# Kernel tuning notes

Hardware: AMD Instinct MI355X
Metric: run time of the kernel (lower is better)

## Reference

```python
import jax, jax.numpy as jnp
import numpy as np

N = 131072        # total points
NUM_SEG = 128     # number of point clouds / segments
INC = 3
HID = 128
OUTC = 128
NUM_LAYER = 6
NUM_INNER = 2
EPS = 1e-3        # ACN eps
CLAMP_MIN = 1e-3  # clamp(min=0.001) on normalizer


def setup_inputs() -> dict:
    key = jax.random.key(0)
    ks = jax.random.split(key, 10)
    s = 0.05
    x = jax.random.normal(ks[0], (N, INC), dtype=jnp.float32)
    segment_idx = jnp.sort(jax.random.randint(ks[1], (N,), 0, NUM_SEG, dtype=jnp.int32))
    weight_pri = jax.random.uniform(ks[2], (N,), dtype=jnp.float32)
    Win0 = jax.random.normal(ks[3], (INC, HID), dtype=jnp.float32) * s
    bin0 = jnp.zeros((HID,), jnp.float32)
    Win_rest = jax.random.normal(ks[4], (4, HID, HID), dtype=jnp.float32) * s
    bin_rest = jnp.zeros((4, HID), jnp.float32)
    # 6 ResBlocks x 2 inner ConvLayers: Linear(128,128) + ACN(att Linear(128,1)) + relu
    conv_W = jax.random.normal(ks[5], (NUM_LAYER, NUM_INNER, HID, HID), dtype=jnp.float32) * s
    conv_b = jnp.zeros((NUM_LAYER, NUM_INNER, HID), jnp.float32)
    att_W = jax.random.normal(ks[6], (NUM_LAYER, NUM_INNER, HID, 1), dtype=jnp.float32) * s
    att_b = jnp.zeros((NUM_LAYER, NUM_INNER, 1), jnp.float32)
    # output Mlp: Linear(128,128)+lrelu, Linear(128,128)
    out_W = jax.random.normal(ks[7], (2, HID, OUTC), dtype=jnp.float32) * s
    out_b = jnp.zeros((2, OUTC), jnp.float32)
    return dict(x=x, segment_idx=segment_idx, weight_pri=weight_pri,
                Win0=Win0, bin0=bin0, Win_rest=Win_rest, bin_rest=bin_rest,
                conv_W=conv_W, conv_b=conv_b, att_W=att_W, att_b=att_b,
                out_W=out_W, out_b=out_b)


def _seg_sum(v, seg):
    return jax.ops.segment_sum(v, seg, num_segments=NUM_SEG)


def _scatter_softmax(att, seg):
    # stable softmax within segments; att: [N, 1]
    m = jax.ops.segment_max(att, seg, num_segments=NUM_SEG)
    e = jnp.exp(att - m[seg])
    return e / _seg_sum(e, seg)[seg]


def _acn(x, aw, ab, seg, wp):
    # attentive context normalization; x: [N, HID]
    a = _scatter_softmax(x @ aw + ab, seg)          # [N, 1]
    a = a * wp[:, None]
    a = a / jnp.clip(_seg_sum(a, seg)[seg], CLAMP_MIN)
    mean = _seg_sum(x * a, seg)[seg]
    out = x - mean
    std = jnp.sqrt(_seg_sum(a * out * out, seg)[seg] + EPS)
    return out / std, a


def reference(x, segment_idx, weight_pri, Win0, bin0, Win_rest, bin_rest,
              conv_W, conv_b, att_W, att_b, out_W, out_b):
    lrelu = jax.nn.leaky_relu  # slope 0.01, matches nn.LeakyReLU default
    # input Mlp + outer leaky_relu in Acne.forward
    h = lrelu(x @ Win0 + bin0)
    for i in range(3):
        h = lrelu(h @ Win_rest[i] + bin_rest[i])
    h = h @ Win_rest[3] + bin_rest[3]
    h = lrelu(h)
    last_a = None
    for li in range(NUM_LAYER):
        xin = h
        for j in range(NUM_INNER):
            xin = xin @ conv_W[li, j] + conv_b[li, j]
            xin, last_a = _acn(xin, att_W[li, j], att_b[li, j], segment_idx, weight_pri)
            xin = jax.nn.relu(xin)
        h = xin + h  # residual
    h = lrelu(h @ out_W[0] + out_b[0])
    h = h @ out_W[1] + out_b[1]
    return h, last_a
```

## Files before the change

kernel.cpp:

```cpp
#include <hip/hip_runtime.h>
#include <hip/hip_cooperative_groups.h>

namespace cg = cooperative_groups;

#define N_PTS 131072
#define NSEG 128
#define SW 132
#define PSTRIDE 33024

typedef unsigned short u16;
typedef __attribute__((ext_vector_type(8))) short short8;
typedef __attribute__((ext_vector_type(8))) unsigned short ushort8;
typedef __attribute__((ext_vector_type(4))) float f32x4;

__device__ __forceinline__ float b2f(u16 u){union{unsigned v;float f;}x;x.v=((unsigned)u)<<16;return x.f;}
__device__ __forceinline__ u16 f2b(float f){unsigned u=__float_as_uint(f);u+=0x7FFFu+((u>>16)&1u);return (u16)(u>>16);}
__device__ __forceinline__ float aload(const float* p){ return __hip_atomic_load(p, __ATOMIC_RELAXED, __HIP_MEMORY_SCOPE_AGENT); }
__device__ __forceinline__ void astore(float* p, float v){ __hip_atomic_store(p, v, __ATOMIC_RELAXED, __HIP_MEMORY_SCOPE_AGENT); }

__global__ __launch_bounds__(256) void k_wpack(const float* __restrict__ Wr,
    const float* __restrict__ convW, const float* __restrict__ outW,
    const float* __restrict__ attW, const float* __restrict__ attb,
    const float* __restrict__ convb,
    u16* __restrict__ Wf, float* __restrict__ uAtt, float* __restrict__ cAtt){
  int mat = blockIdx.x;
  const float* W = (mat<4) ? (Wr+mat*16384) : (mat<16) ? (convW+(mat-4)*16384) : (outW+(mat-16)*16384);
  u16* dst = Wf + mat*16384;
  for (int t = threadIdx.x; t < 16384; t += 256){ int n=t>>7,k=t&127; dst[t]=f2b(W[k*128+n]); }
  if (mat>=4 && mat<16){
    int l = mat-4;
    __syncthreads();
    int tid = threadIdx.x;
    if (tid < 128){
      float s = 0.f;
      for (int c=0;c<128;c++) s += b2f(dst[c*128+tid]) * attW[l*128+c];
      uAtt[l*128+tid] = s;
    } else if (tid == 128){
      float s = attb[l];
      for (int c=0;c<128;c++) s += convb[l*128+c] * attW[l*128+c];
      cAtt[l] = s;
    }
  }
}

__device__ __forceinline__ void gemm_lrelu_inplace(u16* Xs, const u16* __restrict__ Wm,
    const float* __restrict__ Bv, int wave, int q, int m16){
  short8 bfr[2][4];
  const int cA = wave*32 + 2*m16;
  #pragma unroll
  for (int ct=0; ct<2; ct++){
    int n = cA + ct;
    #pragma unroll
    for (int kc=0; kc<4; kc++) bfr[ct][kc] = *(const short8*)&Wm[n*128 + kc*32 + q*8];
  }
  const float b0 = Bv[cA], b1 = Bv[cA+1];
  #pragma unroll
  for (int rt=0; rt<8; rt++){
    const int r0 = rt*16;
    f32x4 a0={0,0,0,0}, a1={0,0,0,0};
    short8 afn = *(const short8*)&Xs[(r0+m16)*SW + q*8];
    #pragma unroll
    for (int kc=0; kc<4; kc++){
      short8 afc = afn;
      if (kc<3) afn = *(const short8*)&Xs[(r0+m16)*SW + (kc+1)*32 + q*8];
      a0 = __builtin_amdgcn_mfma_f32_16x16x32_bf16(afc, bfr[0][kc], a0, 0,0,0);
      a1 = __builtin_amdgcn_mfma_f32_16x16x32_bf16(afc, bfr[1][kc], a1, 0,0,0);
    }
    __syncthreads();
    #pragma unroll
    for (int t=0; t<4; t++){
      int rloc = r0 + q*4 + t;
      float v0 = a0[t]+b0, v1 = a1[t]+b1;
      v0 = v0>0.f ? v0 : 0.01f*v0;
      v1 = v1>0.f ? v1 : 0.01f*v1;
      *(unsigned*)&Xs[rloc*SW + cA] = (unsigned)f2b(v0) | ((unsigned)f2b(v1)<<16);
    }
  }
}

__global__ __launch_bounds__(256, 4) void k_fused(
    const float* __restrict__ x, const int* __restrict__ seg, const float* __restrict__ wp,
    const float* __restrict__ Win0, const float* __restrict__ bin0,
    const float* __restrict__ br, const float* __restrict__ convb, const float* __restrict__ outb,
    const u16* __restrict__ Wf, const float* __restrict__ uAtt, const float* __restrict__ cAtt,
    float* __restrict__ Pstat, float* __restrict__ Of, float* __restrict__ a_out)
{
  __shared__ u16 Xs[128*SW];
  __shared__ float rowP[128];
  __shared__ float eS[128], aS[128];
  __shared__ int   sgS[128];
  __shared__ float wpS[128];
  __shared__ float MhL[2][128], ScL[2][128];

  const int tid=threadIdx.x, wave=tid>>6, lane=tid&63, q=lane>>4, m16=lane&15;
  const int row0=blockIdx.x*128;
  const int c8=(tid*8)&127;
  const int rbase=tid>>4;

  cg::grid_group grid = cg::this_grid();

  if (tid<128){ sgS[tid]=seg[row0+tid]; wpS[tid]=wp[row0+tid]; }
  if (tid<33){ int idx=blockIdx.x*33+tid; if (idx<PSTRIDE) astore(Pstat+idx, 0.f); }
  __syncthreads();

  const int sA=sgS[0], sB=sgS[127];
  const bool uni=(sA==sB);
  unsigned slotm=0;
  #pragma unroll
  for (int i=0;i<8;i++) if (sgS[i*16+rbase]!=sA) slotm|=1u<<i;

  {
    float w0[8],w1[8],w2[8],bv[8];
    *(float4*)&w0[0]=*(const float4*)&Win0[c8];     *(float4*)&w0[4]=*(const float4*)&Win0[c8+4];
    *(float4*)&w1[0]=*(const float4*)&Win0[128+c8]; *(float4*)&w1[4]=*(const float4*)&Win0[128+c8+4];
    *(float4*)&w2[0]=*(const float4*)&Win0[256+c8]; *(float4*)&w2[4]=*(const float4*)&Win0[256+c8+4];
    *(float4*)&bv[0]=*(const float4*)&bin0[c8];     *(float4*)&bv[4]=*(const float4*)&bin0[c8+4];
    #pragma unroll
    for (int i=0;i<8;i++){
      int rloc=i*16+rbase, r=row0+rloc;
      float x0=x[r*3], x1=x[r*3+1], x2=x[r*3+2];
      ushort8 ob;
      #pragma unroll
      for (int jj=0;jj<8;jj++){
        float v=bv[jj]+x0*w0[jj]+x1*w1[jj]+x2*w2[jj];
        v=v>0.f?v:0.01f*v;
        ob[jj]=f2b(v);
      }
      *(ushort8*)&Xs[rloc*SW+c8]=ob;
    }
  }
  __syncthreads();

  #pragma unroll 1
  for (int l=0;l<4;l++){
    gemm_lrelu_inplace(Xs, Wf + (size_t)l*16384, br + l*128, wave,q,m16);
    __syncthreads();
  }

  grid.sync();

  float h[64];

  #pragma unroll 1
  for (int j=0;j<12;j++){
    float* Pw = Pstat + (j%3)*PSTRIDE;
    const float* Pr = Pstat + ((j+2)%3)*PSTRIDE;
    float* Pn = Pstat + ((j+1)%3)*PSTRIDE;

    if (j>0){
      int half=tid>>7, ch=tid&127;
      int s = half ? sB : sA;
      float Z=aload(Pr+s), Wd=aload(Pr+128+s);
      float invd=1.f/fmaxf(Wd, fmaxf(1e-3f*Z, 1e-30f));
      float sa=Wd*invd;
      float m =aload(Pr+256  + s*128+ch)*invd;
      float qv=aload(Pr+16640+ s*128+ch)*invd;
      MhL[half][ch]=m;
      ScL[half][ch]=rsqrtf(qv+(sa-2.f)*m*m+1e-3f);
    }
    float uv[8];
    { float4 u0=*(const float4*)&uAtt[j*128+c8]; float4 u1=*(const float4*)&uAtt[j*128+c8+4];
      uv[0]=u0.x;uv[1]=u0.y;uv[2]=u0.z;uv[3]=u0.w;uv[4]=u1.x;uv[5]=u1.y;uv[6]=u1.z;uv[7]=u1.w; }
    const float cL0 = cAtt[j];
    __syncthreads();

    #pragma unroll
    for (int i=0;i<8;i++){
      const int rloc=i*16+rbase;
      ushort8 raw=*(const ushort8*)&Xs[rloc*SW+c8];
      float v[8];
      if (j==0){
        #pragma unroll
        for (int jj=0;jj<8;jj++){ v[jj]=b2f(raw[jj]); h[i*8+jj]=v[jj]; }
      } else {
        const int sl=(slotm>>i)&1;
        #pragma unroll
        for (int jj=0;jj<8;jj++){
          float vv=(b2f(raw[jj])-MhL[sl][c8+jj])*ScL[sl][c8+jj];
          vv=fmaxf(vv,0.f);
          if ((j&1)==0){ vv+=h[i*8+jj]; h[i*8+jj]=vv; }
          v[jj]=vv;
        }
        ushort8 ob;
        #pragma unroll
        for (int jj=0;jj<8;jj++) ob[jj]=f2b(v[jj]);
        *(ushort8*)&Xs[rloc*SW+c8]=ob;
      }
      float p = v[0]*uv[0]+v[1]*uv[1]+v[2]*uv[2]+v[3]*uv[3]
              + v[4]*uv[4]+v[5]*uv[5]+v[6]*uv[6]+v[7]*uv[7];
      p += __shfl_xor(p,1,64); p += __shfl_xor(p,2,64);
      p += __shfl_xor(p,4,64); p += __shfl_xor(p,8,64);
      if (m16==0) rowP[rloc]=p;
    }
    __syncthreads();

    if (tid<128){
      float l2=rowP[tid]+cL0;
      float e=__expf(fminf(l2,60.f));
      float sw=e*wpS[tid];
      eS[tid]=e; aS[tid]=sw;
    }
    if (tid<33){ int idx=blockIdx.x*33+tid; if (idx<PSTRIDE) astore(Pn+idx, 0.f); }
    __syncthreads();
    if (tid<128){
      int s=sgS[tid];
      if (tid==0 || sgS[tid-1]!=s){
        float se=0.f, ss=0.f;
        for (int i2=tid;i2<128 && sgS[i2]==s;i2++){ se+=eS[i2]; ss+=aS[i2]; }
        atomicAdd(&Pw[s],se); atomicAdd(&Pw[128+s],ss);
      }
    }

    const u16* Wm = Wf + (size_t)(4+j)*16384;
    const float* Bv = convb + j*128;
    short8 bfr[2][4];
    const int cA = wave*32+2*m16;
    #pragma unroll
    for (int ct=0;ct<2;ct++){
      int n=cA+ct;
      #pragma unroll
      for (int kc=0;kc<4;kc++) bfr[ct][kc]=*(const short8*)&Wm[n*128+kc*32+q*8];
    }
    const float bias0=Bv[cA], bias1=Bv[cA+1];
    float* cM=Pw+256; float* cQ=Pw+16640;
    int cur = uni ? sA : sgS[q*4];
    float sx0=0.f,sq0=0.f,sx1=0.f,sq1=0.f;
    #pragma unroll
    for (int rt=0;rt<8;rt++){
      const int r0=rt*16;
      f32x4 a0={0,0,0,0}, a1={0,0,0,0};
      short8 afn=*(const short8*)&Xs[(r0+m16)*SW+q*8];
      #pragma unroll
      for (int kc=0;kc<4;kc++){
        short8 afc=afn;
        if (kc<3) afn=*(const short8*)&Xs[(r0+m16)*SW+(kc+1)*32+q*8];
        a0=__builtin_amdgcn_mfma_f32_16x16x32_bf16(afc,bfr[0][kc],a0,0,0,0);
        a1=__builtin_amdgcn_mfma_f32_16x16x32_bf16(afc,bfr[1][kc],a1,0,0,0);
      }
      __syncthreads();
      #pragma unroll
      for (int t=0;t<4;t++){
        int rloc=r0+q*4+t;
        float v0=a0[t]+bias0, v1=a1[t]+bias1;
        *(unsigned*)&Xs[rloc*SW+cA]=(unsigned)f2b(v0)|((unsigned)f2b(v1)<<16);
        float a=aS[rloc];
        if (!uni){
          int s=sgS[rloc];
          if (s!=cur){
            atomicAdd(&cM[cur*128+cA],sx0);  atomicAdd(&cQ[cur*128+cA],sq0);
            atomicAdd(&cM[cur*128+cA+1],sx1);atomicAdd(&cQ[cur*128+cA+1],sq1);
            sx0=sq0=sx1=sq1=0.f; cur=s;
          }
        }
        sx0+=a*v0; sq0+=a*v0*v0; sx1+=a*v1; sq1+=a*v1*v1;
      }
    }
    if (uni){
      sx0+=__shfl_xor(sx0,16,64); sx0+=__shfl_xor(sx0,32,64);
      sq0+=__shfl_xor(sq0,16,64); sq0+=__shfl_xor(sq0,32,64);
      sx1+=__shfl_xor(sx1,16,64); sx1+=__shfl_xor(sx1,32,64);
      sq1+=__shfl_xor(sq1,16,64); sq1+=__shfl_xor(sq1,32,64);
      if (q==0){
        atomicAdd(&cM[sA*128+cA],sx0);  atomicAdd(&cQ[sA*128+cA],sq0);
        atomicAdd(&cM[sA*128+cA+1],sx1);atomicAdd(&cQ[sA*128+cA+1],sq1);
      }
    } else {
      atomicAdd(&cM[cur*128+cA],sx0);  atomicAdd(&cQ[cur*128+cA],sq0);
      atomicAdd(&cM[cur*128+cA+1],sx1);atomicAdd(&cQ[cur*128+cA+1],sq1);
    }
    grid.sync();
  }

  {
    const float* Pr = Pstat + 2*PSTRIDE;
    { int half=tid>>7, ch=tid&127;
      int s = half ? sB : sA;
      float Z=aload(Pr+s), Wd=aload(Pr+128+s);
      float invd=1.f/fmaxf(Wd, fmaxf(1e-3f*Z, 1e-30f));
      float sa=Wd*invd;
      float m =aload(Pr+256  + s*128+ch)*invd;
      float qv=aload(Pr+16640+ s*128+ch)*invd;
      MhL[half][ch]=m;
      ScL[half][ch]=rsqrtf(qv+(sa-2.f)*m*m+1e-3f);
    }
    if (tid<128){
      int s=sgS[tid];
      float Z=aload(Pr+s), Wd=aload(Pr+128+s);
      float invd=1.f/fmaxf(Wd, fmaxf(1e-3f*Z, 1e-30f));
      a_out[row0+tid]=aS[tid]*invd;
    }
    __syncthreads();
    #pragma unroll
    for (int i=0;i<8;i++){
      const int rloc=i*16+rbase;
      ushort8 raw=*(const ushort8*)&Xs[rloc*SW+c8];
      const int sl=(slotm>>i)&1;
      ushort8 ob;
      #pragma unroll
      for (int jj=0;jj<8;jj++){
        float vv=(b2f(raw[jj])-MhL[sl][c8+jj])*ScL[sl][c8+jj];
        vv=fmaxf(vv,0.f)+h[i*8+jj];
        ob[jj]=f2b(vv);
      }
      *(ushort8*)&Xs[rloc*SW+c8]=ob;
    }
    __syncthreads();
    gemm_lrelu_inplace(Xs, Wf+(size_t)16*16384, outb, wave,q,m16);
    __syncthreads();
    {
      const u16* Wm=Wf+(size_t)17*16384;
      short8 bfr[2][4];
      const int cA=wave*32+2*m16;
      #pragma unroll
      for (int ct=0;ct<2;ct++){
        int n=cA+ct;
        #pragma unroll
        for (int kc=0;kc<4;kc++) bfr[ct][kc]=*(const short8*)&Wm[n*128+kc*32+q*8];
      }
      const float b0=outb[128+cA], b1=outb[128+cA+1];
      #pragma unroll
      for (int rt=0;rt<8;rt++){
        const int r0=rt*16;
        f32x4 a0={0,0,0,0}, a1={0,0,0,0};
        short8 afn=*(const short8*)&Xs[(r0+m16)*SW+q*8];
        #pragma unroll
        for (int kc=0;kc<4;kc++){
          short8 afc=afn;
          if (kc<3) afn=*(const short8*)&Xs[(r0+m16)*SW+(kc+1)*32+q*8];
          a0=__builtin_amdgcn_mfma_f32_16x16x32_bf16(afc,bfr[0][kc],a0,0,0,0);
          a1=__builtin_amdgcn_mfma_f32_16x16x32_bf16(afc,bfr[1][kc],a1,0,0,0);
        }
        #pragma unroll
        for (int t=0;t<4;t++){
          int rloc=r0+q*4+t;
          float2 o={a0[t]+b0, a1[t]+b1};
          ((float2*)Of)[(size_t)(row0+rloc)*64 + wave*16 + m16]=o;
        }
      }
    }
  }
}

__global__ __launch_bounds__(256) void k_zero(float* __restrict__ M0, float* __restrict__ Q0,
                                              float* __restrict__ Z0, float* __restrict__ W0){
  int t = blockIdx.x * 256 + threadIdx.x;
  M0[t] = 0.f; Q0[t] = 0.f;
  if (t < 128) { Z0[t] = 0.f; W0[t] = 0.f; }
}

__global__ __launch_bounds__(256) void k_in0(const float* __restrict__ x,
    const float* __restrict__ W0, const float* __restrict__ b0, u16* __restrict__ Tb){
  int gid = blockIdx.x*256 + threadIdx.x;
  int n = gid>>7, c = gid&127;
  float acc = b0[c] + x[n*3]*W0[c] + x[n*3+1]*W0[128+c] + x[n*3+2]*W0[256+c];
  Tb[gid] = f2b(acc > 0.f ? acc : 0.01f*acc);
}

template<bool WH>
__global__ __launch_bounds__(256) void k_mlp(u16* __restrict__ Tb, float* __restrict__ A0,
    const u16* __restrict__ Wfm, const float* __restrict__ Bv){
  __shared__ u16 Xs[128*SW];
  const int tid=threadIdx.x, wave=tid>>6, lane=tid&63, q=lane>>4, m16=lane&15;
  const int row0=blockIdx.x*128;
  const u16* Xb = Tb + (size_t)row0*128;
  #pragma unroll
  for (int i=0;i<8;i++){
    int e8=i*2048+tid*8; int rloc=e8>>7, c8=e8&127;
    *(ushort8*)&Xs[rloc*SW+c8] = *(const ushort8*)&Xb[rloc*128+c8];
  }
  short8 bfr[2][4];
  #pragma unroll
  for (int ct=0;ct<2;ct++){
    int n = wave*32 + 2*m16 + ct;
    #pragma unroll
    for (int kc=0;kc<4;kc++) bfr[ct][kc] = *(const short8*)&Wfm[n*128+kc*32+q*8];
  }
  const int cA = wave*32 + 2*m16;
  const float bias0=Bv[cA], bias1=Bv[cA+1];
  __syncthreads();
  #pragma unroll
  for (int rt=0;rt<8;rt++){
    int r0=rt*16;
    short8 af[4];
    #pragma unroll
    for (int kc=0;kc<4;kc++) af[kc] = *(const short8*)&Xs[(r0+m16)*SW+kc*32+q*8];
    f32x4 a0={0,0,0,0}, a1={0,0,0,0};
    #pragma unroll
    for (int kc=0;kc<4;kc++){
      a0=__builtin_amdgcn_mfma_f32_16x16x32_bf16(af[kc],bfr[0][kc],a0,0,0,0);
      a1=__builtin_amdgcn_mfma_f32_16x16x32_bf16(af[kc],bfr[1][kc],a1,0,0,0);
    }
    #pragma unroll
    for (int t=0;t<4;t++){
      int rloc=r0+q*4+t;
      float v0=a0[t]+bias0, v1=a1[t]+bias1;
      v0=v0>0.f?v0:0.01f*v0; v1=v1>0.f?v1:0.01f*v1;
      size_t wi=(size_t)(row0+rloc)*64 + wave*16 + m16;
      ((unsigned*)Tb)[wi] = (unsigned)f2b(v0) | ((unsigned)f2b(v1)<<16);
      if (WH) { float2 hh={v0,v1}; ((float2*)A0)[wi]=hh; }
    }
  }
}

template<int IN>
__global__ __launch_bounds__(256) void k_conv(u16* __restrict__ Tb, float* __restrict__ A0,
    const u16* __restrict__ Wfm, const float* __restrict__ Bv,
    const float* __restrict__ uL, const float* __restrict__ cL,
    float* __restrict__ L, const int* __restrict__ seg, const float* __restrict__ wpv,
    const float* __restrict__ pZ, const float* __restrict__ pW,
    const float* __restrict__ pM, const float* __restrict__ pQ,
    float* __restrict__ cZ, float* __restrict__ cW,
    float* __restrict__ cM, float* __restrict__ cQ,
    float* __restrict__ nZ, float* __restrict__ nW,
    float* __restrict__ nM, float* __restrict__ nQ){
  __shared__ u16 Xs[128*SW];
  __shared__ float rowP[128];
  __shared__ float eS[128], aS[128];
  __shared__ int sgS[128];
  const int tid=threadIdx.x, wave=tid>>6, lane=tid&63, q=lane>>4, m16=lane&15;
  const int row0=blockIdx.x*128;

  if (tid<16){ nM[blockIdx.x*16+tid]=0.f; nQ[blockIdx.x*16+tid]=0.f; }
  if (blockIdx.x==0 && tid<128){ nZ[tid]=0.f; nW[tid]=0.f; }

  const int c8 = (tid*8)&127;
  float uv[8];
  { float4 u0=*(const float4*)&uL[c8]; float4 u1=*(const float4*)&uL[c8+4];
    uv[0]=u0.x;uv[1]=u0.y;uv[2]=u0.z;uv[3]=u0.w;uv[4]=u1.x;uv[5]=u1.y;uv[6]=u1.z;uv[7]=u1.w; }

  const u16* Xb = Tb + (size_t)row0*128;
  #pragma unroll
  for (int i=0;i<8;i++){
    int rloc = i*16 + (tid>>4);
    ushort8 raw = *(const ushort8*)&Xb[rloc*128+c8];
    float v[8];
    if (IN==1){
      #pragma unroll
      for (int j=0;j<8;j++) v[j]=b2f(raw[j]);
      *(ushort8*)&Xs[rloc*SW+c8] = raw;
    } else {
      int gr=row0+rloc, s=seg[gr];
      float Z=pZ[s], Wd=pW[s];
      float invd = 1.f/fmaxf(Wd, fmaxf(1e-3f*Z, 1e-30f));
      float sa = Wd*invd;
      float4 mn0=*(const float4*)&pM[s*128+c8];
      float4 mn1=*(const float4*)&pM[s*128+c8+4];
      float4 q0=*(const float4*)&pQ[s*128+c8];
      float4 q1=*(const float4*)&pQ[s*128+c8+4];
      float mn[8]={mn0.x,mn0.y,mn0.z,mn0.w,mn1.x,mn1.y,mn1.z,mn1.w};
      float qv[8]={q0.x,q0.y,q0.z,q0.w,q1.x,q1.y,q1.z,q1.w};
      #pragma unroll
      for (int j=0;j<8;j++){
        float m=mn[j]*invd, m2=qv[j]*invd;
        v[j]=fmaxf((b2f(raw[j])-m)*rsqrtf(m2+(sa-2.f)*m*m+1e-3f),0.f);
      }
      if (IN==3){
        float4 h0=*(const float4*)&A0[(size_t)gr*128+c8];
        float4 h1=*(const float4*)&A0[(size_t)gr*128+c8+4];
        v[0]+=h0.x;v[1]+=h0.y;v[2]+=h0.z;v[3]+=h0.w;
        v[4]+=h1.x;v[5]+=h1.y;v[6]+=h1.z;v[7]+=h1.w;
        float4 w0={v[0],v[1],v[2],v[3]}, w1={v[4],v[5],v[6],v[7]};
        *(float4*)&A0[(size_t)gr*128+c8]=w0;
        *(float4*)&A0[(size_t)gr*128+c8+4]=w1;
      }
      ushort8 ob;
      #pragma unroll
      for (int j=0;j<8;j++) ob[j]=f2b(v[j]);
      *(ushort8*)&Xs[rloc*SW+c8]=ob;
    }
    float p = v[0]*uv[0]+v[1]*uv[1]+v[2]*uv[2]+v[3]*uv[3]
            + v[4]*uv[4]+v[5]*uv[5]+v[6]*uv[6]+v[7]*uv[7];
    p += __shfl_xor(p,1,64); p += __shfl_xor(p,2,64);
    p += __shfl_xor(p,4,64); p += __shfl_xor(p,8,64);
    if (m16==0) rowP[rloc]=p;
  }

  short8 bfr[2][4];
  #pragma unroll
  for (int ct=0;ct<2;ct++){
    int n = wave*32 + 2*m16 + ct;
    #pragma unroll
    for (int kc=0;kc<4;kc++) bfr[ct][kc]=*(const short8*)&Wfm[n*128+kc*32+q*8];
  }
  const int cA = wave*32 + 2*m16;
  const float bias0=Bv[cA], bias1=Bv[cA+1];
  __syncthreads();

  if (tid<128){
    int r=row0+tid;
    float l=rowP[tid]+cL[0];
    float e=__expf(fminf(l,60.f));
    float sw=e*wpv[r];
    L[r]=sw;
    eS[tid]=e; aS[tid]=sw; sgS[tid]=seg[r];
  }
  __syncthreads();
  if (tid<128){
    int s=sgS[tid];
    if (tid==0 || sgS[tid-1]!=s){
      float se=0.f, ss=0.f;
      for (int i=tid;i<128 && sgS[i]==s;i++){ se+=eS[i]; ss+=aS[i]; }
      atomicAdd(&cZ[s],se); atomicAdd(&cW[s],ss);
    }
  }

  const int s0=sgS[0], s127=sgS[127];
  const bool uni = (s0==s127);
  int cur = uni ? s0 : sgS[q*4];
  float sx0=0.f,sq0=0.f,sx1=0.f,sq1=0.f;

  #pragma unroll
  for (int rt=0;rt<8;rt++){
    int r0=rt*16;
    short8 af[4];
    #pragma unroll
    for (int kc=0;kc<4;kc++) af[kc]=*(const short8*)&Xs[(r0+m16)*SW+kc*32+q*8];
    f32x4 a0={0,0,0,0}, a1={0,0,0,0};
    #pragma unroll
    for (int kc=0;kc<4;kc++){
      a0=__builtin_amdgcn_mfma_f32_16x16x32_bf16(af[kc],bfr[0][kc],a0,0,0,0);
      a1=__builtin_amdgcn_mfma_f32_16x16x32_bf16(af[kc],bfr[1][kc],a1,0,0,0);
    }
    #pragma unroll
    for (int t=0;t<4;t++){
      int rloc=r0+q*4+t;
      float v0=a0[t]+bias0, v1=a1[t]+bias1;
      ((unsigned*)Tb)[(size_t)(row0+rloc)*64 + wave*16 + m16] =
          (unsigned)f2b(v0) | ((unsigned)f2b(v1)<<16);
      float a = aS[rloc];
      if (!uni){
        int s = sgS[rloc];
        if (s != cur){
          atomicAdd(&cM[cur*128+cA],sx0);  atomicAdd(&cQ[cur*128+cA],sq0);
          atomicAdd(&cM[cur*128+cA+1],sx1);atomicAdd(&cQ[cur*128+cA+1],sq1);
          sx0=sq0=sx1=sq1=0.f; cur=s;
        }
      }
      sx0 += a*v0; sq0 += a*v0*v0;
      sx1 += a*v1; sq1 += a*v1*v1;
    }
  }
  if (uni){
    sx0 += __shfl_xor(sx0,16,64); sx0 += __shfl_xor(sx0,32,64);
    sq0 += __shfl_xor(sq0,16,64); sq0 += __shfl_xor(sq0,32,64);
    sx1 += __shfl_xor(sx1,16,64); sx1 += __shfl_xor(sx1,32,64);
    sq1 += __shfl_xor(sq1,16,64); sq1 += __shfl_xor(sq1,32,64);
    if (q==0){
      atomicAdd(&cM[s0*128+cA],sx0);  atomicAdd(&cQ[s0*128+cA],sq0);
      atomicAdd(&cM[s0*128+cA+1],sx1);atomicAdd(&cQ[s0*128+cA+1],sq1);
    }
  } else {
    atomicAdd(&cM[cur*128+cA],sx0);  atomicAdd(&cQ[cur*128+cA],sq0);
    atomicAdd(&cM[cur*128+cA+1],sx1);atomicAdd(&cQ[cur*128+cA+1],sq1);
  }
}

__global__ __launch_bounds__(256) void k_megaout(const u16* __restrict__ Tb,
    const float* __restrict__ A0, const u16* __restrict__ Wf16, const float* __restrict__ outbv,
    const int* __restrict__ seg, const float* __restrict__ L,
    const float* __restrict__ pZ, const float* __restrict__ pW,
    const float* __restrict__ pM, const float* __restrict__ pQ,
    float* __restrict__ Of, float* __restrict__ a_out){
  __shared__ u16 buf[2*128*SW];
  const int tid=threadIdx.x, wave=tid>>6, lane=tid&63, q=lane>>4, m16=lane&15;
  const int row0=blockIdx.x*128;
  const u16* Xb = Tb + (size_t)row0*128;
  #pragma unroll
  for (int i=0;i<8;i++){
    int e8=i*2048+tid*8; int rloc=e8>>7, c8=e8&127;
    ushort8 raw=*(const ushort8*)&Xb[rloc*128+c8];
    int gr=row0+rloc, s=seg[gr];
    float Z=pZ[s], Wd=pW[s];
    float invd=1.f/fmaxf(Wd, fmaxf(1e-3f*Z,1e-30f));
    float sa=Wd*invd;
    float4 mn0=*(const float4*)&pM[s*128+c8];
    float4 mn1=*(const float4*)&pM[s*128+c8+4];
    float4 q0=*(const float4*)&pQ[s*128+c8];
    float4 q1=*(const float4*)&pQ[s*128+c8+4];
    float mn[8]={mn0.x,mn0.y,mn0.z,mn0.w,mn1.x,mn1.y,mn1.z,mn1.w};
    float qv[8]={q0.x,q0.y,q0.z,q0.w,q1.x,q1.y,q1.z,q1.w};
    float4 h0=*(const float4*)&A0[(size_t)gr*128+c8];
    float4 h1=*(const float4*)&A0[(size_t)gr*128+c8+4];
    float hv[8]={h0.x,h0.y,h0.z,h0.w,h1.x,h1.y,h1.z,h1.w};
    ushort8 ob;
    #pragma unroll
    for (int j=0;j<8;j++){
      float m=mn[j]*invd, m2=qv[j]*invd;
      ob[j]=f2b(fmaxf((b2f(raw[j])-m)*rsqrtf(m2+(sa-2.f)*m*m+1e-3f),0.f)+hv[j]);
    }
    *(ushort8*)&buf[rloc*SW+c8]=ob;
  }
  if (tid<128){
    int r=row0+tid, s=seg[r];
    float invd=1.f/fmaxf(pW[s], fmaxf(1e-3f*pZ[s],1e-30f));
    a_out[r]=L[r]*invd;
  }
  __syncthreads();
  const int cA=wave*32+2*m16;
  {
    u16* dst=buf+128*SW;
    short8 bfr[2][4];
    #pragma unroll
    for (int ct=0;ct<2;ct++){
      int n=wave*32+2*m16+ct;
      #pragma unroll
      for (int kc=0;kc<4;kc++) bfr[ct][kc]=*(const short8*)&Wf16[n*128+kc*32+q*8];
    }
    float bias0=outbv[cA], bias1=outbv[cA+1];
    #pragma unroll
    for (int rt=0;rt<8;rt++){
      int r0=rt*16;
      short8 af[4];
      #pragma unroll
      for (int kc=0;kc<4;kc++) af[kc]=*(const short8*)&buf[(r0+m16)*SW+kc*32+q*8];
      f32x4 a0={0,0,0,0}, a1={0,0,0,0};
      #pragma unroll
      for (int kc=0;kc<4;kc++){
        a0=__builtin_amdgcn_mfma_f32_16x16x32_bf16(af[kc],bfr[0][kc],a0,0,0,0);
        a1=__builtin_amdgcn_mfma_f32_16x16x32_bf16(af[kc],bfr[1][kc],a1,0,0,0);
      }
      #pragma unroll
      for (int t=0;t<4;t++){
        int rloc=r0+q*4+t;
        float v0=a0[t]+bias0, v1=a1[t]+bias1;
        v0=v0>0.f?v0:0.01f*v0; v1=v1>0.f?v1:0.01f*v1;
        dst[rloc*SW+cA]=f2b(v0);
        dst[rloc*SW+cA+1]=f2b(v1);
      }
    }
  }
  __syncthreads();
  {
    const u16* src=buf+128*SW;
    short8 bfr[2][4];
    #pragma unroll
    for (int ct=0;ct<2;ct++){
      int n=wave*32+2*m16+ct;
      #pragma unroll
      for (int kc=0;kc<4;kc++) bfr[ct][kc]=*(const short8*)&Wf16[16384+n*128+kc*32+q*8];
    }
    float bias0=outbv[128+cA], bias1=outbv[128+cA+1];
    #pragma unroll
    for (int rt=0;rt<8;rt++){
      int r0=rt*16;
      short8 af[4];
      #pragma unroll
      for (int kc=0;kc<4;kc++) af[kc]=*(const short8*)&src[(r0+m16)*SW+kc*32+q*8];
      f32x4 a0={0,0,0,0}, a1={0,0,0,0};
      #pragma unroll
      for (int kc=0;kc<4;kc++){
        a0=__builtin_amdgcn_mfma_f32_16x16x32_bf16(af[kc],bfr[0][kc],a0,0,0,0);
        a1=__builtin_amdgcn_mfma_f32_16x16x32_bf16(af[kc],bfr[1][kc],a1,0,0,0);
      }
      #pragma unroll
      for (int t=0;t<4;t++){
        int rloc=r0+q*4+t;
        float2 o={a0[t]+bias0, a1[t]+bias1};
        ((float2*)Of)[(size_t)(row0+rloc)*64 + wave*16 + m16]=o;
      }
    }
  }
}

extern "C" void kernel_launch(void* const* d_in, const int* in_sizes, int n_in,
                              void* d_out, int out_size, void* d_ws, size_t ws_size,
                              hipStream_t stream){
  (void)in_sizes; (void)n_in; (void)out_size; (void)ws_size;
  const float* x     = (const float*)d_in[0];
  const int*   seg   = (const int*)d_in[1];
  const float* wp    = (const float*)d_in[2];
  const float* Win0  = (const float*)d_in[3];
  const float* bin0  = (const float*)d_in[4];
  const float* Wr    = (const float*)d_in[5];
  const float* br    = (const float*)d_in[6];
  const float* convW = (const float*)d_in[7];
  const float* convb = (const float*)d_in[8];
  const float* attW  = (const float*)d_in[9];
  const float* attb  = (const float*)d_in[10];
  const float* outW  = (const float*)d_in[11];
  const float* outb  = (const float*)d_in[12];

  float* A0 = (float*)d_ws;
  u16*   Tb = (u16*)(A0 + (size_t)N_PTS*128);
  float* L  = (float*)(Tb + (size_t)N_PTS*128);
  float* base = L + N_PTS;
  float* SZ[3], *SWt[3], *SM[3], *SQ[3];
  for (int p=0;p<3;p++){
    SZ[p]  = base + p*PSTRIDE;
    SWt[p] = SZ[p] + 128;
    SM[p]  = SWt[p] + 128;
    SQ[p]  = SM[p] + 16384;
  }
  float* uAtt = base + 3*PSTRIDE;
  float* cAtt = uAtt + 12*128;
  u16*   Wf   = (u16*)(cAtt + 16);

  float* Of    = (float*)d_out;
  float* a_out = (float*)d_out + (size_t)N_PTS*128;

  const int GB = N_PTS/128;

  static int coop = -1;
  if (coop < 0){
    int nb = 0;
    hipError_t e = hipOccupancyMaxActiveBlocksPerMultiprocessor(&nb, (const void*)k_fused, 256, 0);
    int ncu = 0, dev = 0;
    hipGetDevice(&dev);
    hipDeviceProp_t prop;
    if (hipGetDeviceProperties(&prop, dev) == hipSuccess) ncu = prop.multiProcessorCount;
    coop = (e == hipSuccess && ncu > 0 && nb * ncu >= GB) ? 1 : 0;
  }

  k_wpack<<<18,256,0,stream>>>(Wr, convW, outW, attW, attb, convb, Wf, uAtt, cAtt);

  if (coop){
    void* args[] = {(void*)&x,(void*)&seg,(void*)&wp,(void*)&Win0,(void*)&bin0,
                    (void*)&br,(void*)&convb,(void*)&outb,
                    (void*)&Wf,(void*)&uAtt,(void*)&cAtt,(void*)&base,
                    (void*)&Of,(void*)&a_out};
    hipLaunchCooperativeKernel((const void*)k_fused, dim3(GB), dim3(256), args, 0, stream);
    return;
  }

  k_zero<<<64,256,0,stream>>>(SM[0],SQ[0],SZ[0],SWt[0]);
  k_in0<<<N_PTS*128/256,256,0,stream>>>(x, Win0, bin0, Tb);

  for (int i=0;i<3;i++)
    k_mlp<false><<<GB,256,0,stream>>>(Tb, nullptr, Wf+i*16384, br+i*128);
  k_mlp<true><<<GB,256,0,stream>>>(Tb, A0, Wf+3*16384, br+3*128);

  for (int j=0;j<12;j++){
    int wp_ = j%3, rp = (j+2)%3, np = (j+1)%3;
    const u16* Wm = Wf + (size_t)(4+j)*16384;
    const float* uj = uAtt + j*128;
    const float* cj = cAtt + j;
    if (j==0)
      k_conv<1><<<GB,256,0,stream>>>(Tb, nullptr, Wm, convb, uj, cj, L, seg, wp,
          nullptr,nullptr,nullptr,nullptr,
          SZ[wp_],SWt[wp_],SM[wp_],SQ[wp_], SZ[np],SWt[np],SM[np],SQ[np]);
    else if (j&1)
      k_conv<2><<<GB,256,0,stream>>>(Tb, nullptr, Wm, convb+j*128, uj, cj, L, seg, wp,
          SZ[rp],SWt[rp],SM[rp],SQ[rp],
          SZ[wp_],SWt[wp_],SM[wp_],SQ[wp_], SZ[np],SWt[np],SM[np],SQ[np]);
    else
      k_conv<3><<<GB,256,0,stream>>>(Tb, A0, Wm, convb+j*128, uj, cj, L, seg, wp,
          SZ[rp],SWt[rp],SM[rp],SQ[rp],
          SZ[wp_],SWt[wp_],SM[wp_],SQ[wp_], SZ[np],SWt[np],SM[np],SQ[np]);
  }

  k_megaout<<<GB,256,0,stream>>>(Tb, A0, Wf+(size_t)16*16384, outb, seg, L,
                                 SZ[2],SWt[2],SM[2],SQ[2], Of, a_out);
}
```

Before: 729.0 us.

## Replace cooperative grid.sync with custom atomic barrier and pack residual to bf16

```diff
diff --git a/kernel.cpp b/kernel.cpp
--- a/kernel.cpp
+++ b/kernel.cpp
@@ -1,10 +1,8 @@
 #include <hip/hip_runtime.h>
-#include <hip/hip_cooperative_groups.h>
-
-namespace cg = cooperative_groups;
 
 #define N_PTS 131072
 #define NSEG 128
+#define NBLK (N_PTS/128)
 #define SW 132
 #define PSTRIDE 33024
 
@@ -15,15 +13,31 @@
 
 __device__ __forceinline__ float b2f(u16 u){union{unsigned v;float f;}x;x.v=((unsigned)u)<<16;return x.f;}
 __device__ __forceinline__ u16 f2b(float f){unsigned u=__float_as_uint(f);u+=0x7FFFu+((u>>16)&1u);return (u16)(u>>16);}
+__device__ __forceinline__ unsigned pk2(u16 a, u16 b){ return (unsigned)a | ((unsigned)b<<16); }
+__device__ __forceinline__ float lo2f(unsigned u){union{unsigned v;float f;}x;x.v=u<<16;return x.f;}
+__device__ __forceinline__ float hi2f(unsigned u){union{unsigned v;float f;}x;x.v=u&0xFFFF0000u;return x.f;}
 __device__ __forceinline__ float aload(const float* p){ return __hip_atomic_load(p, __ATOMIC_RELAXED, __HIP_MEMORY_SCOPE_AGENT); }
 __device__ __forceinline__ void astore(float* p, float v){ __hip_atomic_store(p, v, __ATOMIC_RELAXED, __HIP_MEMORY_SCOPE_AGENT); }
+
+__device__ __forceinline__ void gbar(unsigned* bar, unsigned target){
+  __threadfence();
+  __syncthreads();
+  if (threadIdx.x==0){
+    __hip_atomic_fetch_add(bar, 1u, __ATOMIC_RELAXED, __HIP_MEMORY_SCOPE_AGENT);
+    while (__hip_atomic_load(bar, __ATOMIC_RELAXED, __HIP_MEMORY_SCOPE_AGENT) < target)
+      __builtin_amdgcn_s_sleep(2);
+  }
+  __syncthreads();
+}
 
 __global__ __launch_bounds__(256) void k_wpack(const float* __restrict__ Wr,
     const float* __restrict__ convW, const float* __restrict__ outW,
     const float* __restrict__ attW, const float* __restrict__ attb,
     const float* __restrict__ convb,
-    u16* __restrict__ Wf, float* __restrict__ uAtt, float* __restrict__ cAtt){
+    u16* __restrict__ Wf, float* __restrict__ uAtt, float* __restrict__ cAtt,
+    unsigned* __restrict__ bar){
   int mat = blockIdx.x;
+  if (mat==0 && threadIdx.x==0) __hip_atomic_store(bar, 0u, __ATOMIC_RELAXED, __HIP_MEMORY_SCOPE_AGENT);
   const float* W = (mat<4) ? (Wr+mat*16384) : (mat<16) ? (convW+(mat-4)*16384) : (outW+(mat-16)*16384);
   u16* dst = Wf + mat*16384;
   for (int t = threadIdx.x; t < 16384; t += 256){ int n=t>>7,k=t&127; dst[t]=f2b(W[k*128+n]); }
@@ -73,7 +87,7 @@
       float v0 = a0[t]+b0, v1 = a1[t]+b1;
       v0 = v0>0.f ? v0 : 0.01f*v0;
       v1 = v1>0.f ? v1 : 0.01f*v1;
-      *(unsigned*)&Xs[rloc*SW + cA] = (unsigned)f2b(v0) | ((unsigned)f2b(v1)<<16);
+      *(unsigned*)&Xs[rloc*SW + cA] = pk2(f2b(v0), f2b(v1));
     }
   }
 }
@@ -83,7 +97,8 @@
     const float* __restrict__ Win0, const float* __restrict__ bin0,
     const float* __restrict__ br, const float* __restrict__ convb, const float* __restrict__ outb,
     const u16* __restrict__ Wf, const float* __restrict__ uAtt, const float* __restrict__ cAtt,
-    float* __restrict__ Pstat, float* __restrict__ Of, float* __restrict__ a_out)
+    float* __restrict__ Pstat, float* __restrict__ Of, float* __restrict__ a_out,
+    unsigned* __restrict__ bar)
 {
   __shared__ u16 Xs[128*SW];
   __shared__ float rowP[128];
@@ -97,8 +112,6 @@
   const int c8=(tid*8)&127;
   const int rbase=tid>>4;
 
-  cg::grid_group grid = cg::this_grid();
-
   if (tid<128){ sgS[tid]=seg[row0+tid]; wpS[tid]=wp[row0+tid]; }
   if (tid<33){ int idx=blockIdx.x*33+tid; if (idx<PSTRIDE) astore(Pstat+idx, 0.f); }
   __syncthreads();
@@ -137,9 +150,9 @@
     __syncthreads();
   }
 
-  grid.sync();
-
-  float h[64];
+  gbar(bar, NBLK);
+
+  unsigned hq[32];
 
   #pragma unroll 1
   for (int j=0;j<12;j++){
@@ -171,19 +184,28 @@
       float v[8];
       if (j==0){
         #pragma unroll
-        for (int jj=0;jj<8;jj++){ v[jj]=b2f(raw[jj]); h[i*8+jj]=v[jj]; }
+        for (int jj=0;jj<8;jj++) v[jj]=b2f(raw[jj]);
+        #pragma unroll
+        for (int k=0;k<4;k++) hq[i*4+k]=pk2((u16)raw[2*k],(u16)raw[2*k+1]);
       } else {
         const int sl=(slotm>>i)&1;
         #pragma unroll
         for (int jj=0;jj<8;jj++){
           float vv=(b2f(raw[jj])-MhL[sl][c8+jj])*ScL[sl][c8+jj];
           vv=fmaxf(vv,0.f);
-          if ((j&1)==0){ vv+=h[i*8+jj]; h[i*8+jj]=vv; }
+          if ((j&1)==0){
+            unsigned hp=hq[i*4+(jj>>1)];
+            vv += (jj&1) ? hi2f(hp) : lo2f(hp);
+          }
           v[jj]=vv;
         }
         ushort8 ob;
         #pragma unroll
         for (int jj=0;jj<8;jj++) ob[jj]=f2b(v[jj]);
+        if ((j&1)==0){
+          #pragma unroll
+          for (int k=0;k<4;k++) hq[i*4+k]=pk2((u16)ob[2*k],(u16)ob[2*k+1]);
+        }
         *(ushort8*)&Xs[rloc*SW+c8]=ob;
       }
       float p = v[0]*uv[0]+v[1]*uv[1]+v[2]*uv[2]+v[3]*uv[3]
@@ -242,7 +264,7 @@
       for (int t=0;t<4;t++){
         int rloc=r0+q*4+t;
         float v0=a0[t]+bias0, v1=a1[t]+bias1;
-        *(unsigned*)&Xs[rloc*SW+cA]=(unsigned)f2b(v0)|((unsigned)f2b(v1)<<16);
+        *(unsigned*)&Xs[rloc*SW+cA]=pk2(f2b(v0),f2b(v1));
         float a=aS[rloc];
         if (!uni){
           int s=sgS[rloc];
@@ -268,7 +290,7 @@
       atomicAdd(&cM[cur*128+cA],sx0);  atomicAdd(&cQ[cur*128+cA],sq0);
       atomicAdd(&cM[cur*128+cA+1],sx1);atomicAdd(&cQ[cur*128+cA+1],sq1);
     }
-    grid.sync();
+    gbar(bar, (unsigned)(2+j)*NBLK);
   }
 
   {
@@ -299,7 +321,8 @@
       #pragma unroll
       for (int jj=0;jj<8;jj++){
         float vv=(b2f(raw[jj])-MhL[sl][c8+jj])*ScL[sl][c8+jj];
-        vv=fmaxf(vv,0.f)+h[i*8+jj];
+        unsigned hp=hq[i*4+(jj>>1)];
+        vv=fmaxf(vv,0.f)+((jj&1)?hi2f(hp):lo2f(hp));
         ob[jj]=f2b(vv);
       }
       *(ushort8*)&Xs[rloc*SW+c8]=ob;
@@ -694,11 +717,12 @@
   float* uAtt = base + 3*PSTRIDE;
   float* cAtt = uAtt + 12*128;
   u16*   Wf   = (u16*)(cAtt + 16);
+  unsigned* bar = (unsigned*)(Wf + (size_t)18*16384);
 
   float* Of    = (float*)d_out;
   float* a_out = (float*)d_out + (size_t)N_PTS*128;
 
-  const int GB = N_PTS/128;
+  const int GB = NBLK;
 
   static int coop = -1;
   if (coop < 0){
@@ -711,13 +735,13 @@
     coop = (e == hipSuccess && ncu > 0 && nb * ncu >= GB) ? 1 : 0;
   }
 
-  k_wpack<<<18,256,0,stream>>>(Wr, convW, outW, attW, attb, convb, Wf, uAtt, cAtt);
+  k_wpack<<<18,256,0,stream>>>(Wr, convW, outW, attW, attb, convb, Wf, uAtt, cAtt, bar);
 
   if (coop){
     void* args[] = {(void*)&x,(void*)&seg,(void*)&wp,(void*)&Win0,(void*)&bin0,
                     (void*)&br,(void*)&convb,(void*)&outb,
                     (void*)&Wf,(void*)&uAtt,(void*)&cAtt,(void*)&base,
-                    (void*)&Of,(void*)&a_out};
+                    (void*)&Of,(void*)&a_out,(void*)&bar};
     hipLaunchCooperativeKernel((const void*)k_fused, dim3(GB), dim3(256), args, 0, stream);
     return;
   }
```

Result: no change. 730.3 us (+0.2%).
